# Optimization experiments

Hardware: AMD Instinct MI355X
Metric: run time of the kernel (lower is better)

## Reference

```python
import jax, jax.numpy as jnp
import numpy as np


def _conv1x1(x, w, b):
    # x: (B,C,H,W), w: (O,C), b: (O,)
    return jnp.einsum('oc,bchw->bohw', w, x) + b[None, :, None, None]


def _avg_pool2(x):
    B, C, H, W = x.shape
    return x.reshape(B, C, H // 2, 2, W // 2, 2).mean(axis=(3, 5))


def setup_inputs() -> dict:
    key = jax.random.key(0)
    B, C, H, W = 8, 64, 64, 64
    ks = jax.random.split(key, 14)
    s = 1.0 / np.sqrt(C)

    def wb(k1, k2):
        return (jax.random.uniform(k1, (C, C), jnp.float32, -s, s),
                jax.random.uniform(k2, (C,), jnp.float32, -s, s))

    w_q, b_q = wb(ks[0], ks[1])
    w_K, b_K = wb(ks[2], ks[3])
    w_V, b_V = wb(ks[4], ks[5])
    w_Q, b_Q = wb(ks[6], ks[7])
    w_k, b_k = wb(ks[8], ks[9])
    w_v, b_v = wb(ks[10], ks[11])
    x = jax.random.normal(ks[12], (B, C, H, W), jnp.float32)
    gamma = jnp.ones((1,), jnp.float32)
    return dict(x=x, w_q=w_q, b_q=b_q, w_K=w_K, b_K=b_K, w_V=w_V, b_V=b_V,
                w_Q=w_Q, b_Q=b_Q, w_k=w_k, b_k=b_k, w_v=w_v, b_v=b_v,
                gamma=gamma)


def reference(x, w_q, b_q, w_K, b_K, w_V, b_V, w_Q, b_Q, w_k, b_k, w_v, b_v, gamma):
    B, C, H, W = x.shape
    N = H * W
    N4 = N // 4

    # Stage 1: pooled queries vs full key/value
    q = _conv1x1(x, w_q, b_q)                      # (B,C,H,W); torch views as (B,C,W,H) but H==W
    qp = _avg_pool2(q).reshape(B, C, N4).transpose(0, 2, 1)   # (B,N/4,C)
    Kf = _conv1x1(x, w_K, b_K).reshape(B, C, N)                # (B,C,N)
    Vf = _conv1x1(x, w_V, b_V).reshape(B, C, N)                # (B,C,N)
    attn = jax.nn.softmax(jnp.einsum('bnc,bcm->bnm', qp, Kf), axis=-1)  # (B,N/4,N)
    out = jnp.einsum('bcm,bnm->bcn', Vf, attn)                 # (B,C,N/4)
    out = out.reshape(B, C, H // 2, W // 2)

    # Stage 2: full queries vs pooled-derived key/value
    Qf = _conv1x1(x, w_Q, b_Q).reshape(B, C, N).transpose(0, 2, 1)  # (B,N,C)
    kp = _conv1x1(out, w_k, b_k).reshape(B, C, N4)                  # (B,C,N/4)
    vp = _conv1x1(out, w_v, b_v).reshape(B, C, N4)                  # (B,C,N/4)
    attn2 = jax.nn.softmax(jnp.einsum('bnc,bcm->bnm', Qf, kp), axis=-1)  # (B,N,N/4)
    out2 = jnp.einsum('bcm,bnm->bcn', vp, attn2).reshape(B, C, H, W)

    return gamma * out2 + x
```

## Files before the change

### kernel.cpp

```cpp
#include <hip/hip_runtime.h>
#include <math.h>


typedef __bf16 bf16;
typedef __attribute__((ext_vector_type(4))) __bf16 bf16x4;
typedef __attribute__((ext_vector_type(8))) __bf16 bf16x8;
typedef __attribute__((ext_vector_type(4))) float f32x4;

__device__ __forceinline__ void gl_lds16(const bf16* g, bf16* l) {
    __builtin_amdgcn_global_load_lds(
        (const __attribute__((address_space(1))) unsigned int*)g,
        (__attribute__((address_space(3))) unsigned int*)l,
        16, 0, 0);
}

__device__ __forceinline__ void proj_wave(
    const bf16* __restrict__ src, int TN,
    const float* __restrict__ W, const float* __restrict__ Bs,
    bf16* __restrict__ Y, int tr, int N, int b, int gn0, int lane)
{
    const int c16 = lane & 15, q4 = lane >> 4;
    bf16x8 wa[4][2];
    #pragma unroll
    for (int to = 0; to < 4; ++to)
        #pragma unroll
        for (int h = 0; h < 2; ++h) {
            const float* wp = W + (16 * to + c16) * 64 + q4 * 8 + 32 * h;
            float4 f0 = *(const float4*)wp;
            float4 f1 = *(const float4*)(wp + 4);
            bf16 tmp[8] = {(bf16)f0.x, (bf16)f0.y, (bf16)f0.z, (bf16)f0.w,
                           (bf16)f1.x, (bf16)f1.y, (bf16)f1.z, (bf16)f1.w};
            wa[to][h] = *(bf16x8*)tmp;
        }
    for (int tn = 0; tn < TN; ++tn) {
        bf16x8 xb0 = *(const bf16x8*)&src[(16 * tn + c16) * 72 + q4 * 8];
        bf16x8 xb1 = *(const bf16x8*)&src[(16 * tn + c16) * 72 + q4 * 8 + 32];
        #pragma unroll
        for (int to = 0; to < 4; ++to) {
            f32x4 acc = (f32x4){0.f, 0.f, 0.f, 0.f};
            acc = __builtin_amdgcn_mfma_f32_16x16x32_bf16(wa[to][0], xb0, acc, 0, 0, 0);
            acc = __builtin_amdgcn_mfma_f32_16x16x32_bf16(wa[to][1], xb1, acc, 0, 0, 0);
            if (tr) {
                float4 b4 = *(const float4*)(Bs + 16 * to + q4 * 4);
                bf16x4 yv;
                yv[0] = (bf16)(acc[0] + b4.x); yv[1] = (bf16)(acc[1] + b4.y);
                yv[2] = (bf16)(acc[2] + b4.z); yv[3] = (bf16)(acc[3] + b4.w);
                *(bf16x4*)(Y + ((size_t)b * N + gn0 + 16 * tn + c16) * 64 + 16 * to + q4 * 4) = yv;
            } else {
                float4 b4 = *(const float4*)(Bs + 16 * to + q4 * 4);
                float bias[4] = {b4.x, b4.y, b4.z, b4.w};
                #pragma unroll
                for (int r = 0; r < 4; ++r)
                    Y[((size_t)b * 64 + 16 * to + q4 * 4 + r) * N + gn0 + 16 * tn + c16] =
                        (bf16)(acc[r] + bias[r]);
            }
        }
    }
}

__global__ __launch_bounds__(512) void prep_kernel(
    const float* __restrict__ x,
    const float* __restrict__ w_K, const float* __restrict__ b_K, bf16* __restrict__ Kt,
    const float* __restrict__ w_Q, const float* __restrict__ b_Q, bf16* __restrict__ Qt,
    const float* __restrict__ w_V, const float* __restrict__ b_V, bf16* __restrict__ Vf,
    const float* __restrict__ w_q, const float* __restrict__ b_q, bf16* __restrict__ qpt)
{
    __shared__ float tile[128 * 65];
    __shared__ __align__(16) bf16 xbT[128 * 72];
    __shared__ __align__(16) bf16 xpb[32 * 72];
    const int t  = threadIdx.x;
    const int h2 = blockIdx.x;
    const int b  = blockIdx.y;
    const int n0 = h2 * 128;

    #pragma unroll
    for (int i = 0; i < 16; ++i) {
        int lin = i * 512 + t;
        int n = lin & 127, c = lin >> 7;
        tile[n * 65 + c] = x[((size_t)b * 64 + c) * 4096 + n0 + n];
    }
    __syncthreads();
    #pragma unroll
    for (int i = 0; i < 2; ++i) {
        int slot = i * 512 + t;
        int n = slot >> 3, c0 = (slot & 7) * 8;
        bf16 tmp[8];
        #pragma unroll
        for (int j = 0; j < 8; ++j) tmp[j] = (bf16)tile[n * 65 + c0 + j];
        *(bf16x8*)&xbT[n * 72 + c0] = *(bf16x8*)tmp;
    }
    if (t < 256) {
        int wp = t & 31, c0 = (t >> 5) * 8;
        bf16 tmp[8];
        #pragma unroll
        for (int j = 0; j < 8; ++j) {
            float a = tile[(2 * wp) * 65 + c0 + j] + tile[(2 * wp + 1) * 65 + c0 + j]
                    + tile[(64 + 2 * wp) * 65 + c0 + j] + tile[(64 + 2 * wp + 1) * 65 + c0 + j];
            tmp[j] = (bf16)(0.25f * a);
        }
        *(bf16x8*)&xpb[wp * 72 + c0] = *(bf16x8*)tmp;
    }
    __syncthreads();

    const int lane = t & 63;
    const int w    = t >> 6;
    if (w < 2) {
        proj_wave(xbT + w * 64 * 72, 4, w_K, b_K, Kt, 1, 4096, b, n0 + w * 64, lane);
    } else if (w < 4) {
        proj_wave(xbT + (w - 2) * 64 * 72, 4, w_Q, b_Q, Qt, 1, 4096, b, n0 + (w - 2) * 64, lane);
    } else if (w < 6) {
        proj_wave(xbT + (w - 4) * 64 * 72, 4, w_V, b_V, Vf, 0, 4096, b, n0 + (w - 4) * 64, lane);
    } else if (w == 6) {
        proj_wave(xpb, 2, w_q, b_q, qpt, 1, 1024, b, h2 * 32, lane);
    }
}

template<int NSPLIT, int MODE>
__global__ __launch_bounds__(256, 3) void flash_kernel(
    const bf16* __restrict__ Qt, const bf16* __restrict__ Kt,
    const bf16* __restrict__ Vn, int NQ, int L,
    bf16* __restrict__ Opart, float* __restrict__ Lbuf,
    float* __restrict__ out_f, const float* __restrict__ resid,
    const float* __restrict__ gamma_p)
{
    const int tid  = threadIdx.x;
    const int lane = tid & 63;
    const int w    = tid >> 6;
    const int c16  = lane & 15;
    const int q4   = lane >> 4;
    const int b    = blockIdx.y;
    const int n0   = blockIdx.x * 128 + w * 32;
    const int s    = (NSPLIT > 1) ? blockIdx.z : 0;
    const int SL   = L / NSPLIT;
    const int k0   = s * SL;
    const int ntiles = SL / 64;

    __shared__ __align__(16) bf16 Ks[2][64 * 64];
    __shared__ __align__(16) bf16 Vs[2][64 * 64];
    __shared__ __align__(16) bf16 Pw[4][32 * 72];

    const int rl8 = lane >> 3;
    const int cg  = ((lane & 7) - rl8) & 7;

    const bf16* Kb = Kt + (size_t)b * L * 64;
    const bf16* Vb = Vn + (size_t)b * 64 * L;

    bf16x8 bq[2][2];
    #pragma unroll
    for (int u = 0; u < 2; ++u) {
        const bf16* qrow = Qt + ((size_t)b * NQ + n0 + 16 * u + c16) * 64 + q4 * 8;
        bq[u][0] = *(const bf16x8*)(qrow);
        bq[u][1] = *(const bf16x8*)(qrow + 32);
    }

    f32x4 O[2][4];
    #pragma unroll
    for (int u = 0; u < 2; ++u)
        #pragma unroll
        for (int g = 0; g < 4; ++g) O[u][g] = (f32x4){0.f, 0.f, 0.f, 0.f};
    float l_acc[2] = {0.f, 0.f};

    #pragma unroll
    for (int j = 0; j < 2; ++j) {
        const int row = 16 * w + 8 * j + rl8;
        gl_lds16(Kb + (size_t)(k0 + row) * 64 + cg * 8, &Ks[0][(16 * w + 8 * j) * 64]);
        gl_lds16(Vb + (size_t)row * L + k0 + cg * 8,    &Vs[0][(16 * w + 8 * j) * 64]);
    }
    __syncthreads();

    for (int it = 0; it < ntiles; ++it) {
        const int buf = it & 1;
        if (it + 1 < ntiles) {
            const int kn = k0 + (it + 1) * 64;
            #pragma unroll
            for (int j = 0; j < 2; ++j) {
                const int row = 16 * w + 8 * j + rl8;
                gl_lds16(Kb + (size_t)(kn + row) * 64 + cg * 8, &Ks[buf ^ 1][(16 * w + 8 * j) * 64]);
                gl_lds16(Vb + (size_t)row * L + kn + cg * 8,    &Vs[buf ^ 1][(16 * w + 8 * j) * 64]);
            }
        }

        f32x4 sv[2][4];
        #pragma unroll
        for (int t = 0; t < 4; ++t) {
            const bf16* krow = &Ks[buf][(16 * t + c16) * 64];
            bf16x8 ak0 = *(const bf16x8*)&krow[((q4 + c16) & 7) * 8];
            bf16x8 ak1 = *(const bf16x8*)&krow[((q4 + 4 + c16) & 7) * 8];
            #pragma unroll
            for (int u = 0; u < 2; ++u) {
                f32x4 z = (f32x4){0.f, 0.f, 0.f, 0.f};
                z = __builtin_amdgcn_mfma_f32_16x16x32_bf16(ak0, bq[u][0], z, 0, 0, 0);
                sv[u][t] = __builtin_amdgcn_mfma_f32_16x16x32_bf16(ak1, bq[u][1], z, 0, 0, 0);
            }
        }

        #pragma unroll
        for (int u = 0; u < 2; ++u) {
            #pragma unroll
            for (int t = 0; t < 4; ++t) {
                #pragma unroll
                for (int r = 0; r < 4; ++r) {
                    float p = __expf(sv[u][t][r]);
                    sv[u][t][r] = p;
                    l_acc[u] += p;
                }
                bf16x4 pv;
                pv[0] = (bf16)sv[u][t][0]; pv[1] = (bf16)sv[u][t][1];
                pv[2] = (bf16)sv[u][t][2]; pv[3] = (bf16)sv[u][t][3];
                *(bf16x4*)&Pw[w][(16 * u + c16) * 72 + 16 * t + 4 * q4] = pv;
            }
        }

        #pragma unroll
        for (int h = 0; h < 2; ++h) {
            bf16x8 pf0 = *(const bf16x8*)&Pw[w][(c16) * 72 + 32 * h + 8 * q4];
            bf16x8 pf1 = *(const bf16x8*)&Pw[w][(16 + c16) * 72 + 32 * h + 8 * q4];
            #pragma unroll
            for (int g = 0; g < 4; ++g) {
                bf16x8 av = *(const bf16x8*)&Vs[buf][(16 * g + c16) * 64 + ((4 * h + q4 + c16) & 7) * 8];
                O[0][g] = __builtin_amdgcn_mfma_f32_16x16x32_bf16(av, pf0, O[0][g], 0, 0, 0);
                O[1][g] = __builtin_amdgcn_mfma_f32_16x16x32_bf16(av, pf1, O[1][g], 0, 0, 0);
            }
        }
        __syncthreads();
    }

    float l_tot[2];
    #pragma unroll
    for (int u = 0; u < 2; ++u) {
        float l = l_acc[u];
        l += __shfl_xor(l, 16);
        l += __shfl_xor(l, 32);
        l_tot[u] = l;
    }

    if (MODE == 2) {
        const float gm = gamma_p[0];
        #pragma unroll
        for (int u = 0; u < 2; ++u) {
            float inv = gm / l_tot[u];
            const int n = n0 + 16 * u + c16;
            #pragma unroll
            for (int g = 0; g < 4; ++g) {
                #pragma unroll
                for (int r = 0; r < 4; ++r) {
                    size_t oidx = ((size_t)b * 64 + 16 * g + 4 * q4 + r) * NQ + n;
                    out_f[oidx] = O[u][g][r] * inv + resid[oidx];
                }
            }
        }
    } else {
        #pragma unroll
        for (int u = 0; u < 2; ++u) {
            float inv = 1.0f / l_tot[u];
            bf16* dst = Opart + ((size_t)(b * NSPLIT + s) * NQ + n0 + 16 * u + c16) * 64 + q4 * 4;
            #pragma unroll
            for (int g = 0; g < 4; ++g) {
                bf16x4 yv;
                #pragma unroll
                for (int r = 0; r < 4; ++r) yv[r] = (bf16)(O[u][g][r] * inv);
                *(bf16x4*)(dst + 16 * g) = yv;
            }
        }
        if (lane < 16) {
            #pragma unroll
            for (int u = 0; u < 2; ++u)
                Lbuf[(b * NSPLIT + s) * NQ + n0 + 16 * u + lane] = l_tot[u];
        }
    }
}

__global__ __launch_bounds__(256) void comb1kv_kernel(
    const bf16* __restrict__ Opart, const float* __restrict__ Lbuf,
    const float* __restrict__ w_k, const float* __restrict__ b_k, bf16* __restrict__ kpt,
    const float* __restrict__ w_v, const float* __restrict__ b_v, bf16* __restrict__ vp)
{
    __shared__ __align__(16) bf16 tile[32 * 72];
    __shared__ float wbuf[32 * 8];
    const int t  = threadIdx.x;
    const int m0 = blockIdx.x * 32;
    const int b  = blockIdx.y;

    if (t < 32) {
        int m = m0 + t;
        float ls[8], lt = 0.f;
        #pragma unroll
        for (int s = 0; s < 8; ++s) {
            ls[s] = Lbuf[(b * 8 + s) * 1024 + m];
            lt += ls[s];
        }
        float inv = 1.f / lt;
        #pragma unroll
        for (int s = 0; s < 8; ++s) wbuf[t * 8 + s] = ls[s] * inv;
    }
    __syncthreads();

    #pragma unroll
    for (int i = 0; i < 2; ++i) {
        int ml = i * 16 + (t >> 4);
        int c4 = (t & 15) * 4;
        const bf16* base = Opart + ((size_t)(b * 8) * 1024 + m0 + ml) * 64 + c4;
        float a0 = 0.f, a1 = 0.f, a2 = 0.f, a3 = 0.f;
        #pragma unroll
        for (int s = 0; s < 8; ++s) {
            bf16x4 v = *(const bf16x4*)(base + (size_t)s * 1024 * 64);
            float wg = wbuf[ml * 8 + s];
            a0 += (float)v[0] * wg; a1 += (float)v[1] * wg;
            a2 += (float)v[2] * wg; a3 += (float)v[3] * wg;
        }
        bf16x4 o; o[0] = (bf16)a0; o[1] = (bf16)a1; o[2] = (bf16)a2; o[3] = (bf16)a3;
        *(bf16x4*)&tile[ml * 72 + c4] = o;
    }
    __syncthreads();

    const int lane = t & 63;
    const int w    = t >> 6;
    const int c16 = lane & 15, q4 = lane >> 4;

    if (w < 2) {
        bf16x8 wb[4][2];
        #pragma unroll
        for (int to = 0; to < 4; ++to)
            #pragma unroll
            for (int h = 0; h < 2; ++h) {
                const float* wp = w_k + (16 * to + c16) * 64 + q4 * 8 + 32 * h;
                float4 f0 = *(const float4*)wp;
                float4 f1 = *(const float4*)(wp + 4);
                bf16 tmp[8] = {(bf16)f0.x, (bf16)f0.y, (bf16)f0.z, (bf16)f0.w,
                               (bf16)f1.x, (bf16)f1.y, (bf16)f1.z, (bf16)f1.w};
                wb[to][h] = *(bf16x8*)tmp;
            }
        const int tm = w;
        bf16x8 a0 = *(const bf16x8*)&tile[(16 * tm + c16) * 72 + q4 * 8];
        bf16x8 a1 = *(const bf16x8*)&tile[(16 * tm + c16) * 72 + q4 * 8 + 32];
        #pragma unroll
        for (int to = 0; to < 4; ++to) {
            f32x4 acc = (f32x4){0.f, 0.f, 0.f, 0.f};
            acc = __builtin_amdgcn_mfma_f32_16x16x32_bf16(a0, wb[to][0], acc, 0, 0, 0);
            acc = __builtin_amdgcn_mfma_f32_16x16x32_bf16(a1, wb[to][1], acc, 0, 0, 0);
            float bias = b_k[16 * to + c16];
            #pragma unroll
            for (int r = 0; r < 4; ++r)
                kpt[((size_t)b * 1024 + m0 + 16 * tm + 4 * q4 + r) * 64 + 16 * to + c16] =
                    (bf16)(acc[r] + bias);
        }
    } else {
        bf16x8 wa[4][2];
        #pragma unroll
        for (int ta = 0; ta < 4; ++ta)
            #pragma unroll
            for (int h = 0; h < 2; ++h) {
                const float* wp = w_v + (16 * ta + c16) * 64 + q4 * 8 + 32 * h;
                float4 f0 = *(const float4*)wp;
                float4 f1 = *(const float4*)(wp + 4);
                bf16 tmp[8] = {(bf16)f0.x, (bf16)f0.y, (bf16)f0.z, (bf16)f0.w,
                               (bf16)f1.x, (bf16)f1.y, (bf16)f1.z, (bf16)f1.w};
                wa[ta][h] = *(bf16x8*)tmp;
            }
        const int tm = w - 2;
        bf16x8 bb0 = *(const bf16x8*)&tile[(16 * tm + c16) * 72 + q4 * 8];
        bf16x8 bb1 = *(const bf16x8*)&tile[(16 * tm + c16) * 72 + q4 * 8 + 32];
        #pragma unroll
        for (int ta = 0; ta < 4; ++ta) {
            f32x4 acc = (f32x4){0.f, 0.f, 0.f, 0.f};
            acc = __builtin_amdgcn_mfma_f32_16x16x32_bf16(wa[ta][0], bb0, acc, 0, 0, 0);
            acc = __builtin_amdgcn_mfma_f32_16x16x32_bf16(wa[ta][1], bb1, acc, 0, 0, 0);
            float4 b4 = *(const float4*)(b_v + 16 * ta + 4 * q4);
            float bias[4] = {b4.x, b4.y, b4.z, b4.w};
            #pragma unroll
            for (int r = 0; r < 4; ++r)
                vp[((size_t)b * 64 + 16 * ta + 4 * q4 + r) * 1024 + m0 + 16 * tm + c16] =
                    (bf16)(acc[r] + bias[r]);
        }
    }
}

extern "C" void kernel_launch(void* const* d_in, const int* in_sizes, int n_in,
                              void* d_out, int out_size, void* d_ws, size_t ws_size,
                              hipStream_t stream) {
    const float* x    = (const float*)d_in[0];
    const float* w_q  = (const float*)d_in[1];
    const float* b_q  = (const float*)d_in[2];
    const float* w_K  = (const float*)d_in[3];
    const float* b_K  = (const float*)d_in[4];
    const float* w_V  = (const float*)d_in[5];
    const float* b_V  = (const float*)d_in[6];
    const float* w_Q  = (const float*)d_in[7];
    const float* b_Q  = (const float*)d_in[8];
    const float* w_k  = (const float*)d_in[9];
    const float* b_k  = (const float*)d_in[10];
    const float* w_v  = (const float*)d_in[11];
    const float* b_v  = (const float*)d_in[12];
    const float* gamma = (const float*)d_in[13];
    float* out = (float*)d_out;

    char* ws = (char*)d_ws;
    bf16*  Kt    = (bf16*)ws;   ws += (size_t)8 * 4096 * 64 * 2;
    bf16*  Qt    = (bf16*)ws;   ws += (size_t)8 * 4096 * 64 * 2;
    bf16*  Vf    = (bf16*)ws;   ws += (size_t)8 * 4096 * 64 * 2;
    bf16*  qpt   = (bf16*)ws;   ws += (size_t)8 * 1024 * 64 * 2;
    bf16*  kpt   = (bf16*)ws;   ws += (size_t)8 * 1024 * 64 * 2;
    bf16*  vp    = (bf16*)ws;   ws += (size_t)8 * 64 * 1024 * 2;
    bf16*  Opart = (bf16*)ws;   ws += (size_t)8 * 8 * 1024 * 64 * 2;
    float* Lb    = (float*)ws;  ws += (size_t)8 * 8 * 1024 * 4;

    prep_kernel<<<dim3(32, 8), 512, 0, stream>>>(
        x, w_K, b_K, Kt, w_Q, b_Q, Qt, w_V, b_V, Vf, w_q, b_q, qpt);

    flash_kernel<8, 1><<<dim3(8, 8, 8), 256, 0, stream>>>(
        qpt, Kt, Vf, 1024, 4096, Opart, Lb, nullptr, nullptr, nullptr);

    comb1kv_kernel<<<dim3(32, 8), 256, 0, stream>>>(
        Opart, Lb, w_k, b_k, kpt, w_v, b_v, vp);

    flash_kernel<1, 2><<<dim3(32, 8, 1), 256, 0, stream>>>(
        Qt, kpt, vp, 4096, 1024, nullptr, nullptr, out, x, gamma);
}
```

Baseline: 139.5 us.

## Double K/V tile depth and replace LDS P staging with cross-lane shuffles

The flash kernel now loads two 64-key sub-tiles per iteration into a doubled double-buffered LDS area, which halves the number of block-wide barriers. The per-wave LDS scratch for the probability matrix is removed: the exponentiated scores are packed to bf16 pairs and redistributed into the MFMA B-operand layout with __shfl. LDS use grows to 64 KB and launch bounds drop from 3 to 2 blocks per CU, trading occupancy for fewer syncs and less LDS traffic.

```diff
diff --git a/kernel.cpp b/kernel.cpp
--- a/kernel.cpp
+++ b/kernel.cpp
@@ -3,9 +3,17 @@
 
 
 typedef __bf16 bf16;
+typedef __attribute__((ext_vector_type(2))) __bf16 bf16x2;
 typedef __attribute__((ext_vector_type(4))) __bf16 bf16x4;
 typedef __attribute__((ext_vector_type(8))) __bf16 bf16x8;
 typedef __attribute__((ext_vector_type(4))) float f32x4;
+
+union Pack2 { unsigned int u; bf16x2 v; };
+union PackU { unsigned int u[4]; bf16x8 v; };
+
+__device__ inline unsigned int pack_bf16(float a, float b) {
+    Pack2 p; p.v = (bf16x2){(bf16)a, (bf16)b}; return p.u;
+}
 
 __device__ __forceinline__ void gl_lds16(const bf16* g, bf16* l) {
     __builtin_amdgcn_global_load_lds(
@@ -116,7 +124,7 @@
 }
 
 template<int NSPLIT, int MODE>
-__global__ __launch_bounds__(256, 3) void flash_kernel(
+__global__ __launch_bounds__(256, 2) void flash_kernel(
     const bf16* __restrict__ Qt, const bf16* __restrict__ Kt,
     const bf16* __restrict__ Vn, int NQ, int L,
     bf16* __restrict__ Opart, float* __restrict__ Lbuf,
@@ -133,14 +141,17 @@
     const int s    = (NSPLIT > 1) ? blockIdx.z : 0;
     const int SL   = L / NSPLIT;
     const int k0   = s * SL;
-    const int ntiles = SL / 64;
-
-    __shared__ __align__(16) bf16 Ks[2][64 * 64];
-    __shared__ __align__(16) bf16 Vs[2][64 * 64];
-    __shared__ __align__(16) bf16 Pw[4][32 * 72];
+    const int npairs = SL / 128;
+
+    __shared__ __align__(16) bf16 Ks[2][2][64 * 64];
+    __shared__ __align__(16) bf16 Vs[2][2][64 * 64];
 
     const int rl8 = lane >> 3;
     const int cg  = ((lane & 7) - rl8) & 7;
+
+    const int lane_a = c16 | (((2 * q4) & 3) << 4);
+    const int lane_b = c16 | (((2 * q4 + 1) & 3) << 4);
+    const bool hi = (q4 >= 2);
 
     const bf16* Kb = Kt + (size_t)b * L * 64;
     const bf16* Vb = Vn + (size_t)b * 64 * L;
@@ -161,65 +172,91 @@
     float l_acc[2] = {0.f, 0.f};
 
     #pragma unroll
-    for (int j = 0; j < 2; ++j) {
-        const int row = 16 * w + 8 * j + rl8;
-        gl_lds16(Kb + (size_t)(k0 + row) * 64 + cg * 8, &Ks[0][(16 * w + 8 * j) * 64]);
-        gl_lds16(Vb + (size_t)row * L + k0 + cg * 8,    &Vs[0][(16 * w + 8 * j) * 64]);
+    for (int sub = 0; sub < 2; ++sub) {
+        const int kt = k0 + sub * 64;
+        #pragma unroll
+        for (int j = 0; j < 2; ++j) {
+            const int row = 16 * w + 8 * j + rl8;
+            gl_lds16(Kb + (size_t)(kt + row) * 64 + cg * 8, &Ks[0][sub][(16 * w + 8 * j) * 64]);
+            gl_lds16(Vb + (size_t)row * L + kt + cg * 8,    &Vs[0][sub][(16 * w + 8 * j) * 64]);
+        }
     }
     __syncthreads();
 
-    for (int it = 0; it < ntiles; ++it) {
+    for (int it = 0; it < npairs; ++it) {
         const int buf = it & 1;
-        if (it + 1 < ntiles) {
-            const int kn = k0 + (it + 1) * 64;
-            #pragma unroll
-            for (int j = 0; j < 2; ++j) {
-                const int row = 16 * w + 8 * j + rl8;
-                gl_lds16(Kb + (size_t)(kn + row) * 64 + cg * 8, &Ks[buf ^ 1][(16 * w + 8 * j) * 64]);
-                gl_lds16(Vb + (size_t)row * L + kn + cg * 8,    &Vs[buf ^ 1][(16 * w + 8 * j) * 64]);
-            }
-        }
-
-        f32x4 sv[2][4];
-        #pragma unroll
-        for (int t = 0; t < 4; ++t) {
-            const bf16* krow = &Ks[buf][(16 * t + c16) * 64];
-            bf16x8 ak0 = *(const bf16x8*)&krow[((q4 + c16) & 7) * 8];
-            bf16x8 ak1 = *(const bf16x8*)&krow[((q4 + 4 + c16) & 7) * 8];
+        if (it + 1 < npairs) {
+            const int kn = k0 + (it + 1) * 128;
+            #pragma unroll
+            for (int sub = 0; sub < 2; ++sub) {
+                const int kt = kn + sub * 64;
+                #pragma unroll
+                for (int j = 0; j < 2; ++j) {
+                    const int row = 16 * w + 8 * j + rl8;
+                    gl_lds16(Kb + (size_t)(kt + row) * 64 + cg * 8, &Ks[buf ^ 1][sub][(16 * w + 8 * j) * 64]);
+                    gl_lds16(Vb + (size_t)row * L + kt + cg * 8,    &Vs[buf ^ 1][sub][(16 * w + 8 * j) * 64]);
+                }
+            }
+        }
+
+        #pragma unroll
+        for (int sub = 0; sub < 2; ++sub) {
+            f32x4 sv[2][4];
+            #pragma unroll
+            for (int t = 0; t < 4; ++t) {
+                const bf16* krow = &Ks[buf][sub][(16 * t + c16) * 64];
+                bf16x8 ak0 = *(const bf16x8*)&krow[((q4 + c16) & 7) * 8];
+                bf16x8 ak1 = *(const bf16x8*)&krow[((q4 + 4 + c16) & 7) * 8];
+                #pragma unroll
+                for (int u = 0; u < 2; ++u) {
+                    f32x4 z = (f32x4){0.f, 0.f, 0.f, 0.f};
+                    z = __builtin_amdgcn_mfma_f32_16x16x32_bf16(ak0, bq[u][0], z, 0, 0, 0);
+                    sv[u][t] = __builtin_amdgcn_mfma_f32_16x16x32_bf16(ak1, bq[u][1], z, 0, 0, 0);
+                }
+            }
+
+            unsigned int pk[2][4][2];
             #pragma unroll
             for (int u = 0; u < 2; ++u) {
-                f32x4 z = (f32x4){0.f, 0.f, 0.f, 0.f};
-                z = __builtin_amdgcn_mfma_f32_16x16x32_bf16(ak0, bq[u][0], z, 0, 0, 0);
-                sv[u][t] = __builtin_amdgcn_mfma_f32_16x16x32_bf16(ak1, bq[u][1], z, 0, 0, 0);
-            }
-        }
-
-        #pragma unroll
-        for (int u = 0; u < 2; ++u) {
-            #pragma unroll
-            for (int t = 0; t < 4; ++t) {
-                #pragma unroll
-                for (int r = 0; r < 4; ++r) {
-                    float p = __expf(sv[u][t][r]);
-                    sv[u][t][r] = p;
-                    l_acc[u] += p;
-                }
-                bf16x4 pv;
-                pv[0] = (bf16)sv[u][t][0]; pv[1] = (bf16)sv[u][t][1];
-                pv[2] = (bf16)sv[u][t][2]; pv[3] = (bf16)sv[u][t][3];
-                *(bf16x4*)&Pw[w][(16 * u + c16) * 72 + 16 * t + 4 * q4] = pv;
-            }
-        }
-
-        #pragma unroll
-        for (int h = 0; h < 2; ++h) {
-            bf16x8 pf0 = *(const bf16x8*)&Pw[w][(c16) * 72 + 32 * h + 8 * q4];
-            bf16x8 pf1 = *(const bf16x8*)&Pw[w][(16 + c16) * 72 + 32 * h + 8 * q4];
-            #pragma unroll
-            for (int g = 0; g < 4; ++g) {
-                bf16x8 av = *(const bf16x8*)&Vs[buf][(16 * g + c16) * 64 + ((4 * h + q4 + c16) & 7) * 8];
-                O[0][g] = __builtin_amdgcn_mfma_f32_16x16x32_bf16(av, pf0, O[0][g], 0, 0, 0);
-                O[1][g] = __builtin_amdgcn_mfma_f32_16x16x32_bf16(av, pf1, O[1][g], 0, 0, 0);
+                #pragma unroll
+                for (int t = 0; t < 4; ++t) {
+                    #pragma unroll
+                    for (int r = 0; r < 4; ++r) {
+                        float p = __expf(sv[u][t][r]);
+                        sv[u][t][r] = p;
+                        l_acc[u] += p;
+                    }
+                    pk[u][t][0] = pack_bf16(sv[u][t][0], sv[u][t][1]);
+                    pk[u][t][1] = pack_bf16(sv[u][t][2], sv[u][t][3]);
+                }
+            }
+
+            #pragma unroll
+            for (int h = 0; h < 2; ++h) {
+                bf16x8 pf[2];
+                #pragma unroll
+                for (int u = 0; u < 2; ++u) {
+                    unsigned xa0 = __shfl((int)pk[u][2 * h][0], lane_a);
+                    unsigned xa1 = __shfl((int)pk[u][2 * h][1], lane_a);
+                    unsigned ya0 = __shfl((int)pk[u][2 * h + 1][0], lane_a);
+                    unsigned ya1 = __shfl((int)pk[u][2 * h + 1][1], lane_a);
+                    unsigned xb0 = __shfl((int)pk[u][2 * h][0], lane_b);
+                    unsigned xb1 = __shfl((int)pk[u][2 * h][1], lane_b);
+                    unsigned yb0 = __shfl((int)pk[u][2 * h + 1][0], lane_b);
+                    unsigned yb1 = __shfl((int)pk[u][2 * h + 1][1], lane_b);
+                    PackU pu;
+                    pu.u[0] = hi ? ya0 : xa0;
+                    pu.u[1] = hi ? ya1 : xa1;
+                    pu.u[2] = hi ? yb0 : xb0;
+                    pu.u[3] = hi ? yb1 : xb1;
+                    pf[u] = pu.v;
+                }
+                #pragma unroll
+                for (int g = 0; g < 4; ++g) {
+                    bf16x8 av = *(const bf16x8*)&Vs[buf][sub][(16 * g + c16) * 64 + ((4 * h + q4 + c16) & 7) * 8];
+                    O[0][g] = __builtin_amdgcn_mfma_f32_16x16x32_bf16(av, pf[0], O[0][g], 0, 0, 0);
+                    O[1][g] = __builtin_amdgcn_mfma_f32_16x16x32_bf16(av, pf[1], O[1][g], 0, 0, 0);
+                }
             }
         }
         __syncthreads();
```

Result: slower. 143.4 us (+2.8%).
